# Kernel optimization log

Measured on AMD Instinct MI355X. Metric: run time of the kernel, lower is better.

Reference implementation:

```python
import jax, jax.numpy as jnp
import numpy as np

B, S, D, H, KP, DK = 4, 2048, 1024, 16, 8, 3
DD = D // H
NEG = -1.0e9


def dense(x, W, b):
    return x @ W + b


def dw_conv_causal(x, w, b):
    # x: [B,S,D], w: [DK,D] per-channel kernel, b: [D]; left pad DK-1 zeros -> VALID conv
    xp = jnp.pad(x, ((0, 0), (DK - 1, 0), (0, 0)))
    y = b
    for t in range(DK):
        y = y + xp[:, t:t + S, :] * w[t]
    return y


def split_heads(x):
    return x.reshape(B, S, H, DD).transpose(0, 2, 1, 3)  # [B,H,S,DD]


def pool_causal(x):
    # left pad KP-1 zeros along seq, avg_pool window=stride=KP, VALID
    xp = jnp.pad(x, ((0, 0), (0, 0), (KP - 1, 0), (0, 0)))
    n = (S - 1) // KP + 1  # TF VALID output length
    return xp[:, :, :n * KP, :].reshape(B, H, n, KP, DD).mean(axis=3)


def forward(q, k, v, Wq, bq, Wk, bk, Wv, bv, Wup, bup, Wc, bc,
            wcq, bcq, wck, bck, wcv, bcv):
    norm = float(DD) ** -0.25
    qh = dense(q, Wq, bq) * norm
    kh = dense(k, Wk, bk) * norm
    vh = dense(v, Wv, bv)
    q_in = split_heads(dw_conv_causal(qh, wcq, bcq))
    k_in = split_heads(dw_conv_causal(kh, wck, bck))
    v_in = split_heads(dw_conv_causal(vh, wcv, bcv))
    qp = pool_causal(q_in)  # [B,H,n,DD]
    kp = pool_causal(k_in)
    vp = pool_causal(v_in)
    n = qp.shape[2]
    mask = NEG * (1.0 - jnp.tril(jnp.ones((n, n), dtype=qp.dtype)))
    logits = jnp.einsum('bhnd,bhmd->bhnm', qp, kp) + mask
    attn = jax.nn.softmax(logits, axis=-1)
    out = jnp.einsum('bhnm,bhmd->bhnd', attn, vp)  # [B,H,n,DD]
    up = jnp.repeat(out, KP, axis=2)[:, :, :S, :]  # upsample + crop
    up = dense(up, Wup, bup)
    merged = up.transpose(0, 2, 1, 3).reshape(B, S, D)
    return dense(merged, Wc, bc)


def setup_inputs() -> dict:
    key = jax.random.key(0)
    ks = jax.random.split(key, 20)
    w = lambda i, shp: jax.random.normal(ks[i], shp, dtype=jnp.float32) * 0.02
    return {
        'q': jax.random.normal(ks[0], (B, S, D), dtype=jnp.float32),
        'k': jax.random.normal(ks[1], (B, S, D), dtype=jnp.float32),
        'v': jax.random.normal(ks[2], (B, S, D), dtype=jnp.float32),
        'Wq': w(3, (D, D)), 'bq': jnp.zeros((D,), jnp.float32),
        'Wk': w(4, (D, D)), 'bk': jnp.zeros((D,), jnp.float32),
        'Wv': w(5, (D, D)), 'bv': jnp.zeros((D,), jnp.float32),
        'Wup': w(6, (DD, DD)), 'bup': jnp.zeros((DD,), jnp.float32),
        'Wc': w(7, (D, D)), 'bc': jnp.zeros((D,), jnp.float32),
        'wcq': w(8, (DK, D)), 'bcq': jnp.zeros((D,), jnp.float32),
        'wck': w(9, (DK, D)), 'bck': jnp.zeros((D,), jnp.float32),
        'wcv': w(10, (DK, D)), 'bcv': jnp.zeros((D,), jnp.float32),
    }


def reference(q, k, v, Wq, bq, Wk, bk, Wv, bv, Wup, bup, Wc, bc,
              wcq, bcq, wck, bck, wcv, bcv):
    return forward(q, k, v, Wq, bq, Wk, bk, Wv, bv, Wup, bup, Wc, bc,
                   wcq, bcq, wck, bck, wcv, bcv)
```

## Files before the change

kernel.cpp:

```cpp
#include <hip/hip_runtime.h>
#include <cstdint>
#include <cstddef>

#define Bc  4
#define Sc  2048
#define Dc  1024
#define Hc  16
#define DDc 64
#define Nc  256

typedef unsigned short u16;
typedef unsigned int   u32;
typedef __bf16 bf16_t;
typedef bf16_t bf16x8 __attribute__((ext_vector_type(8)));
typedef float  f32x4  __attribute__((ext_vector_type(4)));

__device__ __forceinline__ u16 f2bf(float x) {
    u32 u = __float_as_uint(x);
    return (u16)((u + 0x7FFFu + ((u >> 16) & 1u)) >> 16);
}
__device__ __forceinline__ u32 pack2(float a, float b) {
    return (u32)f2bf(a) | ((u32)f2bf(b) << 16);
}
__device__ __forceinline__ uint2 pack4(float4 x) {
    return make_uint2(pack2(x.x, x.y), pack2(x.z, x.w));
}
__device__ __forceinline__ float bf2f(u16 x) {
    return __uint_as_float((u32)x << 16);
}
__device__ __forceinline__ float4 f4add(float4 a, float4 b) {
    return make_float4(a.x + b.x, a.y + b.y, a.z + b.z, a.w + b.w);
}
__device__ __forceinline__ float4 f4sub(float4 a, float4 b) {
    return make_float4(a.x - b.x, a.y - b.y, a.z - b.z, a.w - b.w);
}

__device__ __forceinline__ void gload_lds16(const void* gp, void* lp) {
    __builtin_amdgcn_global_load_lds(
        reinterpret_cast<const __attribute__((address_space(1))) void*>(
            reinterpret_cast<uintptr_t>(gp)),
        reinterpret_cast<__attribute__((address_space(3))) void*>(
            reinterpret_cast<uintptr_t>(lp)),
        16, 0, 0);
}

__device__ __forceinline__ void stage64(const char* src, size_t kb, u16* lds,
                                        int lane, size_t rstride) {
    const int rowoff = lane >> 3;
    const int srcg   = ((lane & 7) ^ (rowoff & 7)) * 16;
    const char* s0 = src + kb + (size_t)srcg;
    #pragma unroll
    for (int i = 0; i < 8; ++i)
        gload_lds16(s0 + (size_t)(8 * i + rowoff) * rstride,
                    (char*)lds + i * 1024);
}

__device__ __forceinline__ void frag_read(const u16* lds, int mi, int quad,
                                          bf16x8 f[4][2]) {
    const int key = mi & 7;
    #pragma unroll
    for (int i = 0; i < 4; ++i)
        #pragma unroll
        for (int kc = 0; kc < 2; ++kc) {
            int g = (kc * 4 + quad) ^ key;
            f[i][kc] = *(const bf16x8*)(lds + (i * 16 + mi) * 64 + g * 8);
        }
}

__global__ __launch_bounds__(256) void prep_wt3(
    const float* __restrict__ Wq, const float* __restrict__ Wk,
    const float* __restrict__ Wv, const float* __restrict__ Wc,
    const float* __restrict__ wcq, const float* __restrict__ wck,
    const float* __restrict__ wcv,
    u16* __restrict__ Wt3, u16* __restrict__ Wtc)
{
    __shared__ float T[64][65];
    const int z = blockIdx.z;
    const float* W = (z == 0) ? Wq : (z == 1) ? Wk : (z == 2) ? Wv : Wc;
    const int k0 = blockIdx.y * 64, n0 = blockIdx.x * 64;
    const int c = threadIdx.x & 63, r4 = threadIdx.x >> 6;
    #pragma unroll
    for (int i = 0; i < 16; ++i) {
        int r = i * 4 + r4;
        T[r][c] = W[(size_t)(k0 + r) * 1024 + n0 + c];
    }
    __syncthreads();
    if (z < 3) {
        const float* wc = (z == 0) ? wcq : (z == 1) ? wck : wcv;
        const float fs = 0.125f * ((z == 2) ? 1.0f : 0.35355339059327373f);
        u16* dst0 = Wt3 + (size_t)z * 3145728;
        #pragma unroll
        for (int i = 0; i < 16; ++i) {
            int r = i * 4 + r4;
            int n = n0 + r;
            float w0 = wc[n], w1 = wc[1024 + n], w2 = wc[2048 + n];
            float s2 = fs * w2, s1 = s2 + fs * w1, s0 = s1 + fs * w0;
            float x = T[c][r];
            u16* dst = dst0 + (size_t)n * 3072 + k0 + c;
            dst[0]    = f2bf(x * s0);
            dst[1024] = f2bf(x * s1);
            dst[2048] = f2bf(x * s2);
        }
    } else {
        #pragma unroll
        for (int i = 0; i < 16; ++i) {
            int r = i * 4 + r4;
            Wtc[(size_t)(n0 + r) * 1024 + k0 + c] = f2bf(T[c][r]);
        }
    }
}

__global__ __launch_bounds__(256) void prep_bias(
    const float* __restrict__ wcq, const float* __restrict__ wck, const float* __restrict__ wcv,
    const float* __restrict__ bcq, const float* __restrict__ bck, const float* __restrict__ bcv,
    const float* __restrict__ bq,  const float* __restrict__ bk,  const float* __restrict__ bv,
    float* __restrict__ biasT)
{
    int gid = blockIdx.x * 256 + threadIdx.x;
    int c = gid & 1023, z = gid >> 10;
    const float* wc    = (z == 0) ? wcq : (z == 1) ? wck : wcv;
    const float* bconv = (z == 0) ? bcq : (z == 1) ? bck : bcv;
    const float* bl    = (z == 0) ? bq  : (z == 1) ? bk  : bv;
    const float nrm = (z == 2) ? 1.0f : 0.35355339059327373f;
    float w0 = wc[c], w1 = wc[1024 + c], w2 = wc[2048 + c];
    float bc_ = bconv[c], bl_ = bl[c];
    float* dst = biasT + (size_t)z * 3072 + c;
    dst[0]    = 0.125f * (bc_ + nrm * bl_ * w2);
    dst[1024] = 0.125f * (8.f * bc_ + nrm * bl_ * (7.f * w0 + 8.f * w1 + 8.f * w2));
    dst[2048] = 0.125f * (8.f * bc_ + nrm * bl_ * 8.f * (w0 + w1 + w2));
}

__global__ __launch_bounds__(256) void stage_kernel(
    const float* __restrict__ q, const float* __restrict__ k,
    const float* __restrict__ v, u16* __restrict__ A3)
{
    int gid = blockIdx.x * 256 + threadIdx.x;
    int c4 = gid & 255, t = (gid >> 8) & 255, b = (gid >> 16) & 3, inp = gid >> 18;
    const float* src = (inp == 0) ? q : (inp == 1) ? k : v;
    const float4* Xb = (const float4*)(src + (size_t)b * Sc * Dc) + c4;
    const float4* Xr = Xb + ((ptrdiff_t)(t << 3) - 9) * 256;

    float4 r[10];
    if (t >= 2) {
        #pragma unroll
        for (int i = 0; i < 10; ++i) r[i] = Xr[(ptrdiff_t)i * 256];
    } else if (t == 1) {
        r[0] = make_float4(0.f, 0.f, 0.f, 0.f);
        #pragma unroll
        for (int i = 1; i < 10; ++i) r[i] = Xr[(ptrdiff_t)i * 256];
    } else {
        #pragma unroll
        for (int i = 0; i < 9; ++i) r[i] = make_float4(0.f, 0.f, 0.f, 0.f);
        r[9] = Xr[(ptrdiff_t)9 * 256];
    }

    float4 A0 = f4add(f4add(f4add(r[0], r[1]), f4add(r[2], r[3])),
                      f4add(f4add(r[4], r[5]), f4add(r[6], r[7])));
    float4 B1 = f4sub(r[8], r[0]);
    float4 B2 = f4sub(r[9], r[1]);

    size_t s0 = (size_t)inp * 3145728 + (size_t)(b * 256 + t) * 3072 + c4 * 4;
    *(uint2*)(A3 + s0)        = pack4(A0);
    *(uint2*)(A3 + s0 + 1024) = pack4(B1);
    *(uint2*)(A3 + s0 + 2048) = pack4(B2);
}

__global__ __launch_bounds__(64) void gemm_qkv(
    const u16* __restrict__ A3, const u16* __restrict__ Wt3,
    const float* __restrict__ biasT,
    u16* __restrict__ qb, u16* __restrict__ kb, u16* __restrict__ vt)
{
    __shared__ __align__(16) u16 S[2][2][4096];

    const int lane = threadIdx.x;
    const int mi   = lane & 15;
    const int quad = lane >> 4;

    const int bid = blockIdx.x;
    const int wg  = (bid & 7) * 96 + (bid >> 3);
    const int z   = wg >> 8;
    const int m0  = ((wg >> 4) & 15) * 64;
    const int n0  = (wg & 15) * 64;

    const char* Ab = (const char*)(A3  + (size_t)z * 3145728) + (size_t)m0 * 6144;
    const char* Bb = (const char*)(Wt3 + (size_t)z * 3145728) + (size_t)n0 * 6144;

    f32x4 acc[4][4];
    #pragma unroll
    for (int i = 0; i < 4; ++i)
        #pragma unroll
        for (int j = 0; j < 4; ++j)
            acc[i][j] = (f32x4){0.f, 0.f, 0.f, 0.f};

    stage64(Ab, 0, S[0][0], lane, 6144);
    stage64(Bb, 0, S[0][1], lane, 6144);

    #pragma unroll 1
    for (int t = 0; t < 48; ++t) {
        const int cur = t & 1;
        if (t < 47) {
            stage64(Ab, (size_t)(t + 1) * 128, S[cur ^ 1][0], lane, 6144);
            stage64(Bb, (size_t)(t + 1) * 128, S[cur ^ 1][1], lane, 6144);
            asm volatile("s_waitcnt vmcnt(16)" ::: "memory");
        } else {
            asm volatile("s_waitcnt vmcnt(0)" ::: "memory");
        }
        __builtin_amdgcn_sched_barrier(0);

        bf16x8 af[4][2], bf[4][2];
        frag_read(S[cur][0], mi, quad, af);
        frag_read(S[cur][1], mi, quad, bf);

        #pragma unroll
        for (int kc = 0; kc < 2; ++kc)
            #pragma unroll
            for (int i = 0; i < 4; ++i)
                #pragma unroll
                for (int j = 0; j < 4; ++j)
                    acc[i][j] = __builtin_amdgcn_mfma_f32_16x16x32_bf16(af[i][kc], bf[j][kc], acc[i][j], 0, 0, 0);
    }

    const float* bT = biasT + (size_t)z * 3072;
    if (z == 2) {
        #pragma unroll
        for (int j = 0; j < 4; ++j) {
            const int col = n0 + j * 16 + mi;
            const int h = col >> 6, d = col & 63;
            #pragma unroll
            for (int i = 0; i < 4; ++i) {
                const int row = m0 + i * 16 + quad * 4;
                const int b = row >> 8, t0 = row & 255;
                const int bh = b * 16 + h;
                u16 w[4];
                #pragma unroll
                for (int r = 0; r < 4; ++r) {
                    int t = t0 + r;
                    w[r] = f2bf(acc[i][j][r] + bT[(t < 2 ? t : 2) * 1024 + col]);
                }
                *(uint2*)(vt + (size_t)bh * 20480 + (size_t)d * 256 + t0) =
                    make_uint2((u32)w[0] | ((u32)w[1] << 16), (u32)w[2] | ((u32)w[3] << 16));
            }
        }
    } else {
        u16* dst = z ? kb : qb;
        #pragma unroll
        for (int j = 0; j < 4; ++j) {
            const int col = n0 + j * 16 + mi;
            const int h = col >> 6, d = col & 63;
            #pragma unroll
            for (int i = 0; i < 4; ++i) {
                const int row = m0 + i * 16 + quad * 4;
                const int b = row >> 8;
                const int bh = b * 16 + h;
                #pragma unroll
                for (int r = 0; r < 4; ++r) {
                    int t = (row & 255) + r;
                    dst[(((size_t)bh * 256 + t) << 6) + d] =
                        f2bf(acc[i][j][r] + bT[(t < 2 ? t : 2) * 1024 + col]);
                }
            }
        }
    }
}

__global__ __launch_bounds__(256) void vpad_kernel(u16* __restrict__ vt)
{
    const int bh = blockIdx.x;
    const int tid = threadIdx.x;
    const int rr = tid >> 4;
    const int c0 = (tid & 15) * 16;
    u32 fill = (rr == 0) ? 0x3F803F80u : 0u;
    uint4 val = make_uint4(fill, fill, fill, fill);
    uint4* p = (uint4*)(vt + (size_t)bh * 80 * 256 + (size_t)(64 + rr) * 256 + c0);
    p[0] = val;
    p[1] = val;
}

__global__ __launch_bounds__(64) void attn_mfma(
    const u16* __restrict__ qb, const u16* __restrict__ kb,
    const u16* __restrict__ vt, float* __restrict__ ao)
{
    __shared__ __align__(16) u16 P[64 * 72];
    const int qt   = blockIdx.x;
    const int bh   = blockIdx.y;
    const int lane = threadIdx.x;
    const int mi   = lane & 15;
    const int quad = lane >> 4;

    const u16* Qb = qb + (((size_t)bh * 256 + qt * 64) << 6);
    const u16* Kb = kb + ((size_t)bh << 14);
    const u16* Vt = vt + (size_t)bh * 80 * 256;

    bf16x8 qf[4][2];
    #pragma unroll
    for (int it = 0; it < 4; ++it)
        #pragma unroll
        for (int kc = 0; kc < 2; ++kc)
            qf[it][kc] = *(const bf16x8*)(Qb + ((it * 16 + mi) << 6) + kc * 32 + quad * 8);

    f32x4 o[4][5];
    #pragma unroll
    for (int it = 0; it < 4; ++it)
        #pragma unroll
        for (int jn = 0; jn < 5; ++jn)
            o[it][jn] = (f32x4){0.f, 0.f, 0.f, 0.f};

    for (int kt = 0; kt <= qt; ++kt) {
        bf16x8 kf[4][2];
        #pragma unroll
        for (int jt = 0; jt < 4; ++jt)
            #pragma unroll
            for (int kc = 0; kc < 2; ++kc)
                kf[jt][kc] = *(const bf16x8*)(Kb + ((kt * 64 + jt * 16 + mi) << 6) + kc * 32 + quad * 8);

        f32x4 s[4][4];
        #pragma unroll
        for (int it = 0; it < 4; ++it)
            #pragma unroll
            for (int jt = 0; jt < 4; ++jt)
                s[it][jt] = (f32x4){0.f, 0.f, 0.f, 0.f};
        #pragma unroll
        for (int kc = 0; kc < 2; ++kc)
            #pragma unroll
            for (int it = 0; it < 4; ++it)
                #pragma unroll
                for (int jt = 0; jt < 4; ++jt)
                    s[it][jt] = __builtin_amdgcn_mfma_f32_16x16x32_bf16(qf[it][kc], kf[jt][kc], s[it][jt], 0, 0, 0);

        const bool diag = (kt == qt);
        #pragma unroll
        for (int it = 0; it < 4; ++it)
            #pragma unroll
            for (int jt = 0; jt < 4; ++jt)
                #pragma unroll
                for (int r = 0; r < 4; ++r) {
                    int qrow = it * 16 + quad * 4 + r;
                    int kcol = jt * 16 + mi;
                    float e = __expf(s[it][jt][r]);
                    if (diag && kcol > qrow) e = 0.f;
                    P[qrow * 72 + kcol] = f2bf(e);
                }

        bf16x8 pf[4][2];
        #pragma unroll
        for (int it = 0; it < 4; ++it)
            #pragma unroll
            for (int kc = 0; kc < 2; ++kc)
                pf[it][kc] = *(const bf16x8*)(P + (it * 16 + mi) * 72 + kc * 32 + quad * 8);

        bf16x8 vf[5][2];
        #pragma unroll
        for (int jn = 0; jn < 5; ++jn)
            #pragma unroll
            for (int kc = 0; kc < 2; ++kc)
                vf[jn][kc] = *(const bf16x8*)(Vt + (size_t)(jn * 16 + mi) * 256 + kt * 64 + kc * 32 + quad * 8);

        #pragma unroll
        for (int kc = 0; kc < 2; ++kc)
            #pragma unroll
            for (int it = 0; it < 4; ++it)
                #pragma unroll
                for (int jn = 0; jn < 5; ++jn)
                    o[it][jn] = __builtin_amdgcn_mfma_f32_16x16x32_bf16(pf[it][kc], vf[jn][kc], o[it][jn], 0, 0, 0);
    }

    #pragma unroll
    for (int it = 0; it < 4; ++it) {
        float inv[4];
        #pragma unroll
        for (int r = 0; r < 4; ++r) {
            float lv = __shfl(o[it][4][r], (lane & 48));
            inv[r] = 1.0f / lv;
        }
        #pragma unroll
        for (int jn = 0; jn < 4; ++jn)
            #pragma unroll
            for (int r = 0; r < 4; ++r) {
                int row = qt * 64 + it * 16 + quad * 4 + r;
                ao[(((size_t)bh * 256 + row) << 6) + jn * 16 + mi] = o[it][jn][r] * inv[r];
            }
    }
}

__global__ __launch_bounds__(256) void updense_kernel(
    const float* __restrict__ ao, const float* __restrict__ Wup,
    const float* __restrict__ bup, u16* __restrict__ ms)
{
    __shared__ float Ws[64 * 64];
    __shared__ float rows[4 * 64];
    const int tid = threadIdx.x;

    #pragma unroll
    for (int i = 0; i < 4; ++i)
        ((float4*)Ws)[tid + 256 * i] = ((const float4*)Wup)[tid + 256 * i];
    rows[tid] = ao[(size_t)blockIdx.x * 256 + tid];
    __syncthreads();

    const int r = tid >> 6, dp = tid & 63;
    const int R = blockIdx.x * 4 + r;
    const int b = R >> 12;
    const int h = (R >> 8) & 15;
    const int m = R & 255;

    float acc = bup[dp];
    #pragma unroll
    for (int d = 0; d < 64; ++d)
        acc += rows[r * 64 + d] * Ws[d * 64 + dp];

    ms[((size_t)(b * Nc + m) << 10) + h * 64 + dp] = f2bf(acc);
}

__global__ __launch_bounds__(64) void gemm_out(
    const u16* __restrict__ A, const u16* __restrict__ Bt,
    const float* __restrict__ bias, float* __restrict__ C)
{
    __shared__ __align__(16) u16 S[2][2][4096];

    const int lane = threadIdx.x;
    const int mi   = lane & 15;
    const int quad = lane >> 4;

    const int bid = blockIdx.x;
    const int wg  = (bid & 7) * 32 + (bid >> 3);
    const int m0  = (wg >> 4) * 64;
    const int n0  = (wg & 15) * 64;

    const char* Ab = (const char*)A  + (size_t)m0 * 2048;
    const char* Bb = (const char*)Bt + (size_t)n0 * 2048;

    f32x4 acc[4][4];
    #pragma unroll
    for (int i = 0; i < 4; ++i)
        #pragma unroll
        for (int j = 0; j < 4; ++j)
            acc[i][j] = (f32x4){0.f, 0.f, 0.f, 0.f};

    stage64(Ab, 0, S[0][0], lane, 2048);
    stage64(Bb, 0, S[0][1], lane, 2048);

    #pragma unroll 1
    for (int t = 0; t < 16; ++t) {
        const int cur = t & 1;
        if (t < 15) {
            stage64(Ab, (size_t)(t + 1) * 128, S[cur ^ 1][0], lane, 2048);
            stage64(Bb, (size_t)(t + 1) * 128, S[cur ^ 1][1], lane, 2048);
            asm volatile("s_waitcnt vmcnt(16)" ::: "memory");
        } else {
            asm volatile("s_waitcnt vmcnt(0)" ::: "memory");
        }
        __builtin_amdgcn_sched_barrier(0);

        bf16x8 af[4][2], bf[4][2];
        frag_read(S[cur][0], mi, quad, af);
        frag_read(S[cur][1], mi, quad, bf);

        #pragma unroll
        for (int kc = 0; kc < 2; ++kc)
            #pragma unroll
            for (int i = 0; i < 4; ++i)
                #pragma unroll
                for (int j = 0; j < 4; ++j)
                    acc[i][j] = __builtin_amdgcn_mfma_f32_16x16x32_bf16(af[i][kc], bf[j][kc], acc[i][j], 0, 0, 0);
    }

    #pragma unroll
    for (int j = 0; j < 4; ++j) {
        const int col = n0 + j * 16 + mi;
        const float bv = bias[col];
        #pragma unroll
        for (int i = 0; i < 4; ++i) {
            const int row = m0 + i * 16 + quad * 4;
            #pragma unroll
            for (int r = 0; r < 4; ++r)
                C[(size_t)(row + r) * 1024 + col] = acc[i][j][r] + bv;
        }
    }
}

__global__ __launch_bounds__(256) void upsample_kernel(
    const float* __restrict__ C, float* __restrict__ out)
{
    const float4* C4  = (const float4*)C;
    float4*       out4 = (float4*)out;
    int idx0 = blockIdx.x * 1024 + threadIdx.x;
    #pragma unroll
    for (int rep = 0; rep < 4; ++rep) {
        int o4   = idx0 + rep * 256;
        int col4 = o4 & 255;
        int rowo = o4 >> 8;
        int b    = rowo >> 11;
        int tc   = (rowo & 2047) >> 3;
        out4[o4] = C4[(size_t)((b << 8) + tc) * 256 + col4];
    }
}

extern "C" void kernel_launch(void* const* d_in, const int* in_sizes, int n_in,
                              void* d_out, int out_size, void* d_ws, size_t ws_size,
                              hipStream_t stream) {
    const float* q   = (const float*)d_in[0];
    const float* k   = (const float*)d_in[1];
    const float* v   = (const float*)d_in[2];
    const float* Wq  = (const float*)d_in[3];
    const float* bq  = (const float*)d_in[4];
    const float* Wk  = (const float*)d_in[5];
    const float* bk  = (const float*)d_in[6];
    const float* Wv  = (const float*)d_in[7];
    const float* bv  = (const float*)d_in[8];
    const float* Wup = (const float*)d_in[9];
    const float* bup = (const float*)d_in[10];
    const float* Wc  = (const float*)d_in[11];
    const float* bc  = (const float*)d_in[12];
    const float* wcq = (const float*)d_in[13];
    const float* bcq = (const float*)d_in[14];
    const float* wck = (const float*)d_in[15];
    const float* bck = (const float*)d_in[16];
    const float* wcv = (const float*)d_in[17];
    const float* bcv = (const float*)d_in[18];

    u16* A3 = (u16*)d_out;

    char* wsb = (char*)d_ws;
    u16*   Wt3   = (u16*)wsb;
    u16*   Wtc   = (u16*)(wsb + 18874368);
    float* biasT = (float*)(wsb + 20971520);
    u16*   qb    = (u16*)(wsb + 21008384);
    u16*   kb    = (u16*)(wsb + 23105536);
    u16*   vt    = (u16*)(wsb + 25202688);
    float* ao    = (float*)(wsb + 27824128);
    u16*   ms    = (u16*)(wsb + 32018432);
    float* Cf    = ao;

    prep_wt3<<<dim3(16, 16, 4), 256, 0, stream>>>(Wq, Wk, Wv, Wc, wcq, wck, wcv, Wt3, Wtc);
    prep_bias<<<12, 256, 0, stream>>>(wcq, wck, wcv, bcq, bck, bcv, bq, bk, bv, biasT);
    stage_kernel<<<3072, 256, 0, stream>>>(q, k, v, A3);
    gemm_qkv<<<768, 64, 0, stream>>>(A3, Wt3, biasT, qb, kb, vt);
    vpad_kernel<<<64, 256, 0, stream>>>(vt);
    attn_mfma<<<dim3(4, 64), 64, 0, stream>>>(qb, kb, vt, ao);
    updense_kernel<<<(Bc * Hc * Nc) / 4, 256, 0, stream>>>(ao, Wup, bup, ms);
    gemm_out<<<256, 64, 0, stream>>>(ms, Wtc, bc, Cf);
    upsample_kernel<<<2048, 256, 0, stream>>>(Cf, (float*)d_out);
}
```

Before: 257.1 us.

## Merge prep kernels, fold vpad into gemm_qkv, fuse upsample into output GEMM

Combines the weight-transpose, bias-prep and input-staging kernels into one launch with block-range dispatch. Moves the v-padding fill into extra blocks of the QKV GEMM launch. The output GEMM now stages its tile in LDS and writes each row eight times directly to the final output, removing the intermediate C buffer and the separate upsample kernel. This cuts launch count and a full intermediate round trip through global memory. In exchange the output GEMM gets a larger LDS footprint and a long serial store loop over only 256 single-wave blocks.

```diff
diff --git a/kernel.cpp b/kernel.cpp
--- a/kernel.cpp
+++ b/kernel.cpp
@@ -67,74 +67,76 @@
         }
 }
 
-__global__ __launch_bounds__(256) void prep_wt3(
+__global__ __launch_bounds__(256) void prep_stage(
+    const float* __restrict__ q,  const float* __restrict__ k,  const float* __restrict__ v,
     const float* __restrict__ Wq, const float* __restrict__ Wk,
     const float* __restrict__ Wv, const float* __restrict__ Wc,
-    const float* __restrict__ wcq, const float* __restrict__ wck,
-    const float* __restrict__ wcv,
-    u16* __restrict__ Wt3, u16* __restrict__ Wtc)
-{
-    __shared__ float T[64][65];
-    const int z = blockIdx.z;
-    const float* W = (z == 0) ? Wq : (z == 1) ? Wk : (z == 2) ? Wv : Wc;
-    const int k0 = blockIdx.y * 64, n0 = blockIdx.x * 64;
-    const int c = threadIdx.x & 63, r4 = threadIdx.x >> 6;
-    #pragma unroll
-    for (int i = 0; i < 16; ++i) {
-        int r = i * 4 + r4;
-        T[r][c] = W[(size_t)(k0 + r) * 1024 + n0 + c];
-    }
-    __syncthreads();
-    if (z < 3) {
-        const float* wc = (z == 0) ? wcq : (z == 1) ? wck : wcv;
-        const float fs = 0.125f * ((z == 2) ? 1.0f : 0.35355339059327373f);
-        u16* dst0 = Wt3 + (size_t)z * 3145728;
-        #pragma unroll
-        for (int i = 0; i < 16; ++i) {
-            int r = i * 4 + r4;
-            int n = n0 + r;
-            float w0 = wc[n], w1 = wc[1024 + n], w2 = wc[2048 + n];
-            float s2 = fs * w2, s1 = s2 + fs * w1, s0 = s1 + fs * w0;
-            float x = T[c][r];
-            u16* dst = dst0 + (size_t)n * 3072 + k0 + c;
-            dst[0]    = f2bf(x * s0);
-            dst[1024] = f2bf(x * s1);
-            dst[2048] = f2bf(x * s2);
-        }
-    } else {
-        #pragma unroll
-        for (int i = 0; i < 16; ++i) {
-            int r = i * 4 + r4;
-            Wtc[(size_t)(n0 + r) * 1024 + k0 + c] = f2bf(T[c][r]);
-        }
-    }
-}
-
-__global__ __launch_bounds__(256) void prep_bias(
     const float* __restrict__ wcq, const float* __restrict__ wck, const float* __restrict__ wcv,
     const float* __restrict__ bcq, const float* __restrict__ bck, const float* __restrict__ bcv,
     const float* __restrict__ bq,  const float* __restrict__ bk,  const float* __restrict__ bv,
-    float* __restrict__ biasT)
+    u16* __restrict__ Wt3, u16* __restrict__ Wtc, float* __restrict__ biasT,
+    u16* __restrict__ A3)
 {
-    int gid = blockIdx.x * 256 + threadIdx.x;
-    int c = gid & 1023, z = gid >> 10;
-    const float* wc    = (z == 0) ? wcq : (z == 1) ? wck : wcv;
-    const float* bconv = (z == 0) ? bcq : (z == 1) ? bck : bcv;
-    const float* bl    = (z == 0) ? bq  : (z == 1) ? bk  : bv;
-    const float nrm = (z == 2) ? 1.0f : 0.35355339059327373f;
-    float w0 = wc[c], w1 = wc[1024 + c], w2 = wc[2048 + c];
-    float bc_ = bconv[c], bl_ = bl[c];
-    float* dst = biasT + (size_t)z * 3072 + c;
-    dst[0]    = 0.125f * (bc_ + nrm * bl_ * w2);
-    dst[1024] = 0.125f * (8.f * bc_ + nrm * bl_ * (7.f * w0 + 8.f * w1 + 8.f * w2));
-    dst[2048] = 0.125f * (8.f * bc_ + nrm * bl_ * 8.f * (w0 + w1 + w2));
-}
-
-__global__ __launch_bounds__(256) void stage_kernel(
-    const float* __restrict__ q, const float* __restrict__ k,
-    const float* __restrict__ v, u16* __restrict__ A3)
-{
-    int gid = blockIdx.x * 256 + threadIdx.x;
+    __shared__ float T[64][65];
+    const int bid = blockIdx.x;
+    const int tid = threadIdx.x;
+
+    if (bid < 1024) {
+        const int z = bid >> 8;
+        const float* W = (z == 0) ? Wq : (z == 1) ? Wk : (z == 2) ? Wv : Wc;
+        const int k0 = ((bid >> 4) & 15) * 64, n0 = (bid & 15) * 64;
+        const int c = tid & 63, r4 = tid >> 6;
+        #pragma unroll
+        for (int i = 0; i < 16; ++i) {
+            int r = i * 4 + r4;
+            T[r][c] = W[(size_t)(k0 + r) * 1024 + n0 + c];
+        }
+        __syncthreads();
+        if (z < 3) {
+            const float* wc = (z == 0) ? wcq : (z == 1) ? wck : wcv;
+            const float fs = 0.125f * ((z == 2) ? 1.0f : 0.35355339059327373f);
+            u16* dst0 = Wt3 + (size_t)z * 3145728;
+            #pragma unroll
+            for (int i = 0; i < 16; ++i) {
+                int r = i * 4 + r4;
+                int n = n0 + r;
+                float w0 = wc[n], w1 = wc[1024 + n], w2 = wc[2048 + n];
+                float s2 = fs * w2, s1 = s2 + fs * w1, s0 = s1 + fs * w0;
+                float x = T[c][r];
+                u16* dst = dst0 + (size_t)n * 3072 + k0 + c;
+                dst[0]    = f2bf(x * s0);
+                dst[1024] = f2bf(x * s1);
+                dst[2048] = f2bf(x * s2);
+            }
+        } else {
+            #pragma unroll
+            for (int i = 0; i < 16; ++i) {
+                int r = i * 4 + r4;
+                Wtc[(size_t)(n0 + r) * 1024 + k0 + c] = f2bf(T[c][r]);
+            }
+        }
+        return;
+    }
+
+    if (bid < 1036) {
+        int gid = (bid - 1024) * 256 + tid;
+        int c = gid & 1023, z = gid >> 10;
+        const float* wc    = (z == 0) ? wcq : (z == 1) ? wck : wcv;
+        const float* bconv = (z == 0) ? bcq : (z == 1) ? bck : bcv;
+        const float* bl    = (z == 0) ? bq  : (z == 1) ? bk  : bv;
+        const float nrm = (z == 2) ? 1.0f : 0.35355339059327373f;
+        float w0 = wc[c], w1 = wc[1024 + c], w2 = wc[2048 + c];
+        float bc_ = bconv[c], bl_ = bl[c];
+        float* dst = biasT + (size_t)z * 3072 + c;
+        dst[0]    = 0.125f * (bc_ + nrm * bl_ * w2);
+        dst[1024] = 0.125f * (8.f * bc_ + nrm * bl_ * (7.f * w0 + 8.f * w1 + 8.f * w2));
+        dst[2048] = 0.125f * (8.f * bc_ + nrm * bl_ * 8.f * (w0 + w1 + w2));
+        return;
+    }
+
+    int sbid0 = bid - 1036;
+    int sbid  = (sbid0 & 7) * 384 + (sbid0 >> 3);
+    int gid = sbid * 256 + tid;
     int c4 = gid & 255, t = (gid >> 8) & 255, b = (gid >> 16) & 3, inp = gid >> 18;
     const float* src = (inp == 0) ? q : (inp == 1) ? k : v;
     const float4* Xb = (const float4*)(src + (size_t)b * Sc * Dc) + c4;
@@ -173,10 +175,29 @@
     __shared__ __align__(16) u16 S[2][2][4096];
 
     const int lane = threadIdx.x;
+    const int bid = blockIdx.x;
+
+    if (bid >= 768) {
+        const int vb = bid - 768;
+        #pragma unroll
+        for (int bh4 = 0; bh4 < 4; ++bh4) {
+            const int bh = vb * 4 + bh4;
+            #pragma unroll
+            for (int it = 0; it < 8; ++it) {
+                int gidx = it * 64 + lane;
+                int row  = 64 + (gidx >> 5);
+                int c0   = (gidx & 31) * 8;
+                u32 fill = (row == 64) ? 0x3F803F80u : 0u;
+                *(uint4*)(vt + (size_t)bh * 20480 + (size_t)row * 256 + c0) =
+                    make_uint4(fill, fill, fill, fill);
+            }
+        }
+        return;
+    }
+
     const int mi   = lane & 15;
     const int quad = lane >> 4;
 
-    const int bid = blockIdx.x;
     const int wg  = (bid & 7) * 96 + (bid >> 3);
     const int z   = wg >> 8;
     const int m0  = ((wg >> 4) & 15) * 64;
@@ -261,19 +282,6 @@
             }
         }
     }
-}
-
-__global__ __launch_bounds__(256) void vpad_kernel(u16* __restrict__ vt)
-{
-    const int bh = blockIdx.x;
-    const int tid = threadIdx.x;
-    const int rr = tid >> 4;
-    const int c0 = (tid & 15) * 16;
-    u32 fill = (rr == 0) ? 0x3F803F80u : 0u;
-    uint4 val = make_uint4(fill, fill, fill, fill);
-    uint4* p = (uint4*)(vt + (size_t)bh * 80 * 256 + (size_t)(64 + rr) * 256 + c0);
-    p[0] = val;
-    p[1] = val;
 }
 
 __global__ __launch_bounds__(64) void attn_mfma(
@@ -410,11 +418,12 @@
     ms[((size_t)(b * Nc + m) << 10) + h * 64 + dp] = f2bf(acc);
 }
 
-__global__ __launch_bounds__(64) void gemm_out(
+__global__ __launch_bounds__(64) void gemm_out_up(
     const u16* __restrict__ A, const u16* __restrict__ Bt,
-    const float* __restrict__ bias, float* __restrict__ C)
+    const float* __restrict__ bias, float* __restrict__ out)
 {
     __shared__ __align__(16) u16 S[2][2][4096];
+    __shared__ __align__(16) float Cs[64][68];
 
     const int lane = threadIdx.x;
     const int mi   = lane & 15;
@@ -465,32 +474,24 @@
 
     #pragma unroll
     for (int j = 0; j < 4; ++j) {
-        const int col = n0 + j * 16 + mi;
-        const float bv = bias[col];
-        #pragma unroll
-        for (int i = 0; i < 4; ++i) {
-            const int row = m0 + i * 16 + quad * 4;
+        const float bv = bias[n0 + j * 16 + mi];
+        #pragma unroll
+        for (int i = 0; i < 4; ++i)
             #pragma unroll
             for (int r = 0; r < 4; ++r)
-                C[(size_t)(row + r) * 1024 + col] = acc[i][j][r] + bv;
-        }
-    }
-}
-
-__global__ __launch_bounds__(256) void upsample_kernel(
-    const float* __restrict__ C, float* __restrict__ out)
-{
-    const float4* C4  = (const float4*)C;
-    float4*       out4 = (float4*)out;
-    int idx0 = blockIdx.x * 1024 + threadIdx.x;
-    #pragma unroll
-    for (int rep = 0; rep < 4; ++rep) {
-        int o4   = idx0 + rep * 256;
-        int col4 = o4 & 255;
-        int rowo = o4 >> 8;
-        int b    = rowo >> 11;
-        int tc   = (rowo & 2047) >> 3;
-        out4[o4] = C4[(size_t)((b << 8) + tc) * 256 + col4];
+                Cs[i * 16 + quad * 4 + r][j * 16 + mi] = acc[i][j][r] + bv;
+    }
+
+    const int col4 = lane & 15;
+    #pragma unroll 4
+    for (int it = 0; it < 128; ++it) {
+        const int crow = it >> 1;
+        const int rep  = ((it & 1) << 2) + (lane >> 4);
+        float4 val = *(const float4*)&Cs[crow][col4 * 4];
+        const int R = m0 + crow;
+        const int b = R >> 8, tc = R & 255;
+        float* po = out + (((size_t)((b << 11) + (tc << 3) + rep)) << 10) + n0 + (col4 << 2);
+        *(float4*)po = val;
     }
 }
 
@@ -528,15 +529,12 @@
     u16*   vt    = (u16*)(wsb + 25202688);
     float* ao    = (float*)(wsb + 27824128);
     u16*   ms    = (u16*)(wsb + 32018432);
-    float* Cf    = ao;
-
-    prep_wt3<<<dim3(16, 16, 4), 256, 0, stream>>>(Wq, Wk, Wv, Wc, wcq, wck, wcv, Wt3, Wtc);
-    prep_bias<<<12, 256, 0, stream>>>(wcq, wck, wcv, bcq, bck, bcv, bq, bk, bv, biasT);
-    stage_kernel<<<3072, 256, 0, stream>>>(q, k, v, A3);
-    gemm_qkv<<<768, 64, 0, stream>>>(A3, Wt3, biasT, qb, kb, vt);
-    vpad_kernel<<<64, 256, 0, stream>>>(vt);
+
+    prep_stage<<<4108, 256, 0, stream>>>(q, k, v, Wq, Wk, Wv, Wc,
+                                         wcq, wck, wcv, bcq, bck, bcv,
+                                         bq, bk, bv, Wt3, Wtc, biasT, A3);
+    gemm_qkv<<<784, 64, 0, stream>>>(A3, Wt3, biasT, qb, kb, vt);
     attn_mfma<<<dim3(4, 64), 64, 0, stream>>>(qb, kb, vt, ao);
     updense_kernel<<<(Bc * Hc * Nc) / 4, 256, 0, stream>>>(ao, Wup, bup, ms);
-    gemm_out<<<256, 64, 0, stream>>>(ms, Wtc, bc, Cf);
-    upsample_kernel<<<2048, 256, 0, stream>>>(Cf, (float*)d_out);
-}
+    gemm_out_up<<<256, 64, 0, stream>>>(ms, Wtc, bc, (float*)d_out);
+}
```

New measurement: 250.5 us. -2.5%, faster.
